# Kernel tuning notes

Measured on AMD Instinct MI355X. Metric: run time of the kernel, lower is better.

Reference implementation:

```python
import jax, jax.numpy as jnp
import numpy as np

N_OBJ = 4096      # n_objects (fixed node count; fc1 consumes flattened node features)
F_IN = 256        # in_feats
H = 256           # n_hidden
C = 128           # n_classes
NE = 8            # number of edge types
EPT = 131072      # edges per etype (avg in-degree 32)


def setup_inputs() -> dict:
    key = jax.random.key(0)
    ks = jax.random.split(key, 16)
    s = 0.02  # weight init scale
    inp = {
        "feat": jax.random.normal(ks[0], (N_OBJ, F_IN), dtype=jnp.float32),
        "edges": jax.random.randint(ks[1], (NE, 2, EPT), 0, N_OBJ, dtype=jnp.int64),
        # 3 hetero layers: layer0 (F_IN->H), layers 1,2 (H->H), each with per-etype Linear
        "W0": jax.random.normal(ks[2], (NE, H, F_IN), dtype=jnp.float32) * s,
        "b0": jnp.zeros((NE, H), dtype=jnp.float32),
        "W1": jax.random.normal(ks[3], (NE, H, H), dtype=jnp.float32) * s,
        "b1": jnp.zeros((NE, H), dtype=jnp.float32),
        "W2": jax.random.normal(ks[4], (NE, H, H), dtype=jnp.float32) * s,
        "b2": jnp.zeros((NE, H), dtype=jnp.float32),
        "fc1_w": jax.random.normal(ks[5], (H, N_OBJ * H), dtype=jnp.float32) * 0.002,
        "fc1_b": jnp.zeros((H,), dtype=jnp.float32),
        "fc2_w": jax.random.normal(ks[6], (C, H), dtype=jnp.float32) * s,
        "fc2_b": jnp.zeros((C,), dtype=jnp.float32),
    }
    return inp


def _hetero_layer(h, W, b, edges):
    # Per-etype linear: Wh[e] = h @ W[e].T + b[e]   -> [NE, N, H]
    Wh = jnp.einsum('nf,ehf->enh', h, W) + b[:, None, :]

    def per_etype(wh, src, dst):
        msg = wh[src]                                            # gather: [EPT, H]
        ssum = jax.ops.segment_sum(msg, dst, num_segments=N_OBJ)  # [N, H]
        deg = jax.ops.segment_sum(jnp.ones_like(dst, dtype=wh.dtype), dst,
                                  num_segments=N_OBJ)             # [N]
        return ssum / jnp.maximum(deg, 1.0)[:, None]              # mean reduce

    agg = jax.vmap(per_etype)(Wh, edges[:, 0], edges[:, 1])  # [NE, N, H]
    # multi_update_all cross-type aggregator 'sum', then activation (relu)
    return jax.nn.relu(agg.sum(axis=0))


def reference(feat, edges, W0, b0, W1, b1, W2, b2, fc1_w, fc1_b, fc2_w, fc2_b):
    h = _hetero_layer(feat, W0, b0, edges)
    h = _hetero_layer(h, W1, b1, edges)
    h = _hetero_layer(h, W2, b2, edges)
    flat = h.reshape(-1)                          # [N*H]
    z = jax.nn.relu(fc1_w @ flat + fc1_b)         # [H]
    out = jax.nn.sigmoid(fc2_w @ z + fc2_b)       # [C]
    return out
```

## Files before the change

### kernel.cpp

```cpp
#include <hip/hip_runtime.h>
#include <math.h>

#define N_OBJ 4096
#define F     256
#define NE    8
#define EPT   131072
#define KCAT  (NE * F)
#define C_OUT 128
#define FC1_K (N_OBJ * F)
#define FCH   16384
#define FNCH  (FC1_K / FCH)
#define FRJ   8

typedef __attribute__((ext_vector_type(8))) short s8v;
typedef __attribute__((ext_vector_type(4))) float f4v;

__device__ inline float bf2f(unsigned short u) {
    unsigned int x = ((unsigned int)u) << 16;
    return __builtin_bit_cast(float, x);
}
__device__ inline unsigned short f2bf(float f) {
    unsigned int x = __builtin_bit_cast(unsigned int, f);
    x += 0x7fff + ((x >> 16) & 1);
    return (unsigned short)(x >> 16);
}
__device__ __forceinline__ int swz(int row, int k8) {
    return (row * 64 + k8 * 8) ^ ((row & 7) << 3);
}


__global__ __launch_bounds__(256) void k_count_deg(const int* __restrict__ edges,
                                                   int* __restrict__ deg) {
    int gid = blockIdx.x * 256 + threadIdx.x;
    int e = gid >> 17;
    int i = gid & (EPT - 1);
    int dst = edges[(e * 2 + 1) * EPT + i];
    atomicAdd(&deg[e * N_OBJ + dst], 1);
}

__global__ __launch_bounds__(256) void k_scan(const int* __restrict__ deg,
                                              int* __restrict__ rowptr,
                                              int* __restrict__ cursor,
                                              float* __restrict__ invdeg) {
    int e = blockIdx.x;
    int t = threadIdx.x;
    __shared__ int part[256];
    int local[16];
    int base = e * N_OBJ + t * 16;
    int s = 0;
#pragma unroll
    for (int i = 0; i < 16; ++i) { local[i] = deg[base + i]; s += local[i]; }
    part[t] = s;
    __syncthreads();
    for (int off = 1; off < 256; off <<= 1) {
        int v = (t >= off) ? part[t - off] : 0;
        __syncthreads();
        part[t] += v;
        __syncthreads();
    }
    int run = part[t] - s;
#pragma unroll
    for (int i = 0; i < 16; ++i) {
        rowptr[base + i] = run;
        cursor[base + i] = run;
        invdeg[base + i] = 1.0f / fmaxf((float)local[i], 1.0f);
        run += local[i];
    }
}

__global__ __launch_bounds__(256) void k_fill(const int* __restrict__ edges,
                                              int* __restrict__ cursor,
                                              int* __restrict__ col) {
    int gid = blockIdx.x * 256 + threadIdx.x;
    int e = gid >> 17;
    int i = gid & (EPT - 1);
    int src = edges[(e * 2 + 0) * EPT + i];
    int dst = edges[(e * 2 + 1) * EPT + i];
    int pos = atomicAdd(&cursor[e * N_OBJ + dst], 1);
    col[e * EPT + pos] = src;
}

__global__ __launch_bounds__(256) void k_bmask(const int* __restrict__ deg,
                                               unsigned int* __restrict__ bmask) {
    int n = blockIdx.x * 256 + threadIdx.x;
    unsigned int m = 0;
#pragma unroll
    for (int e = 0; e < NE; ++e) m |= (deg[e * N_OBJ + n] > 0) ? (1u << e) : 0u;
    bmask[n] = m;
}

#define WQ4 (NE * F * F / 4)
#define FQ4 (N_OBJ * F / 4)
__global__ __launch_bounds__(256) void k_cvt_all(const float* __restrict__ W0,
                                                 const float* __restrict__ W1,
                                                 const float* __restrict__ W2,
                                                 const float* __restrict__ feat,
                                                 unsigned short* __restrict__ Wb0,
                                                 unsigned short* __restrict__ Wb1,
                                                 unsigned short* __restrict__ Wb2,
                                                 unsigned short* __restrict__ featb) {
    int i = blockIdx.x * 256 + threadIdx.x;
    const float* s;
    unsigned short* d;
    int j;
    if (i < WQ4)            { s = W0;   d = Wb0;   j = i; }
    else if (i < 2 * WQ4)   { s = W1;   d = Wb1;   j = i - WQ4; }
    else if (i < 3 * WQ4)   { s = W2;   d = Wb2;   j = i - 2 * WQ4; }
    else                    { s = feat; d = featb; j = i - 3 * WQ4; }
    float4 v = ((const float4*)s)[j];
    ushort4 o;
    o.x = f2bf(v.x); o.y = f2bf(v.y); o.z = f2bf(v.z); o.w = f2bf(v.w);
    ((ushort4*)d)[j] = o;
}

__global__ __launch_bounds__(256) void k_aggregate(const unsigned short* __restrict__ h_in,
                                                   const int* __restrict__ rowptr,
                                                   const int* __restrict__ deg,
                                                   const int* __restrict__ col,
                                                   const float* __restrict__ invdeg,
                                                   unsigned short* __restrict__ ah) {
    int wid = blockIdx.x * 4 + (threadIdx.x >> 6);
    int lane = threadIdx.x & 63;
    int e = wid >> 12;
    int n = wid & (N_OBJ - 1);
    int beg = rowptr[wid];
    int cnt = deg[wid];
    const int* cl = col + e * EPT + beg;
    const ushort4* h4 = (const ushort4*)h_in;
    float a0 = 0.f, a1 = 0.f, a2 = 0.f, a3 = 0.f;
    int k = 0;
    for (; k + 8 <= cnt; k += 8) {
        int s0 = cl[k],     s1 = cl[k + 1], s2 = cl[k + 2], s3 = cl[k + 3];
        int s4 = cl[k + 4], s5 = cl[k + 5], s6 = cl[k + 6], s7 = cl[k + 7];
        ushort4 v0 = h4[s0 * 64 + lane];
        ushort4 v1 = h4[s1 * 64 + lane];
        ushort4 v2 = h4[s2 * 64 + lane];
        ushort4 v3 = h4[s3 * 64 + lane];
        ushort4 v4 = h4[s4 * 64 + lane];
        ushort4 v5 = h4[s5 * 64 + lane];
        ushort4 v6 = h4[s6 * 64 + lane];
        ushort4 v7 = h4[s7 * 64 + lane];
        a0 += bf2f(v0.x) + bf2f(v1.x) + bf2f(v2.x) + bf2f(v3.x)
            + bf2f(v4.x) + bf2f(v5.x) + bf2f(v6.x) + bf2f(v7.x);
        a1 += bf2f(v0.y) + bf2f(v1.y) + bf2f(v2.y) + bf2f(v3.y)
            + bf2f(v4.y) + bf2f(v5.y) + bf2f(v6.y) + bf2f(v7.y);
        a2 += bf2f(v0.z) + bf2f(v1.z) + bf2f(v2.z) + bf2f(v3.z)
            + bf2f(v4.z) + bf2f(v5.z) + bf2f(v6.z) + bf2f(v7.z);
        a3 += bf2f(v0.w) + bf2f(v1.w) + bf2f(v2.w) + bf2f(v3.w)
            + bf2f(v4.w) + bf2f(v5.w) + bf2f(v6.w) + bf2f(v7.w);
    }
    for (; k < cnt; ++k) {
        ushort4 v = h4[cl[k] * 64 + lane];
        a0 += bf2f(v.x); a1 += bf2f(v.y); a2 += bf2f(v.z); a3 += bf2f(v.w);
    }
    float sc = invdeg[wid];
    ushort4 o;
    o.x = f2bf(a0 * sc); o.y = f2bf(a1 * sc); o.z = f2bf(a2 * sc); o.w = f2bf(a3 * sc);
    ((ushort4*)ah)[n * (KCAT / 4) + e * (F / 4) + lane] = o;
}

template <int OUTBF>
__global__ __launch_bounds__(256, 4) void k_gemm(const unsigned short* __restrict__ A,
                                                 const unsigned short* __restrict__ Wb,
                                                 const float* __restrict__ bias,
                                                 const unsigned int* __restrict__ bmask,
                                                 void* __restrict__ Cout) {
    __shared__ short As[2][64 * 64];
    __shared__ short Bs[2][64 * 64];
    int m0 = blockIdx.x * 64, n0 = blockIdx.y * 64;
    int t = threadIdx.x;
    int wave = t >> 6, lane = t & 63;
    int r = lane & 15, g = lane >> 4;
    int row0 = t >> 3, seg0 = t & 7;
    int row1 = row0 + 32;
    int wA0 = swz(row0, seg0), wA1 = swz(row1, seg0);

    const short* Ap = (const short*)A;
    const short* Wp = (const short*)Wb;
    const short* arp0 = Ap + (size_t)(m0 + row0) * KCAT + seg0 * 8;
    const short* arp1 = Ap + (size_t)(m0 + row1) * KCAT + seg0 * 8;
    int brow0 = (n0 + row0) * F + seg0 * 8;
    int brow1 = (n0 + row1) * F + seg0 * 8;

    f4v acc[4];
#pragma unroll
    for (int i = 0; i < 4; ++i) acc[i] = (f4v){0.f, 0.f, 0.f, 0.f};

    {
        s8v a0 = *(const s8v*)(arp0);
        s8v a1 = *(const s8v*)(arp1);
        s8v b0 = *(const s8v*)(Wp + brow0);
        s8v b1 = *(const s8v*)(Wp + brow1);
        *(s8v*)&As[0][wA0] = a0; *(s8v*)&As[0][wA1] = a1;
        *(s8v*)&Bs[0][wA0] = b0; *(s8v*)&Bs[0][wA1] = b1;
    }
    __syncthreads();
#pragma unroll 1
    for (int ks = 0; ks < 32; ++ks) {
        int cur = ks & 1;
        s8v a0, a1, b0, b1;
        if (ks < 31) {
            int kb = (ks + 1) * 64;
            int woff = ((kb >> 8) << 16) + (kb & 255);
            a0 = *(const s8v*)(arp0 + kb);
            a1 = *(const s8v*)(arp1 + kb);
            b0 = *(const s8v*)(Wp + woff + brow0);
            b1 = *(const s8v*)(Wp + woff + brow1);
        }
        const short* as = As[cur];
        const short* bs = Bs[cur];
#pragma unroll
        for (int kk = 0; kk < 2; ++kk) {
            s8v af = *(const s8v*)&as[swz(wave * 16 + r, kk * 4 + g)];
#pragma unroll
            for (int n = 0; n < 4; ++n) {
                s8v bf = *(const s8v*)&bs[swz(n * 16 + r, kk * 4 + g)];
                acc[n] = __builtin_amdgcn_mfma_f32_16x16x32_bf16(af, bf, acc[n], 0, 0, 0);
            }
        }
        if (ks < 31) {
            *(s8v*)&As[cur ^ 1][wA0] = a0; *(s8v*)&As[cur ^ 1][wA1] = a1;
            *(s8v*)&Bs[cur ^ 1][wA0] = b0; *(s8v*)&Bs[cur ^ 1][wA1] = b1;
        }
        __syncthreads();
    }
    int mb = m0 + wave * 16 + g * 4;
    unsigned int msk[4];
#pragma unroll
    for (int reg = 0; reg < 4; ++reg) msk[reg] = bmask[mb + reg];
#pragma unroll
    for (int n = 0; n < 4; ++n) {
        int coln = n0 + n * 16 + r;
        float bcol[NE];
#pragma unroll
        for (int e = 0; e < NE; ++e) bcol[e] = bias[e * F + coln];
#pragma unroll
        for (int reg = 0; reg < 4; ++reg) {
            float v = acc[n][reg];
#pragma unroll
            for (int e = 0; e < NE; ++e)
                if ((msk[reg] >> e) & 1) v += bcol[e];
            v = fmaxf(v, 0.f);
            if (OUTBF) ((unsigned short*)Cout)[(size_t)(mb + reg) * F + coln] = f2bf(v);
            else       ((float*)Cout)[(size_t)(mb + reg) * F + coln] = v;
        }
    }
}

__global__ __launch_bounds__(256) void k_fc1(const float* __restrict__ Wf,
                                             const float* __restrict__ flat,
                                             float* __restrict__ zpart) {
    __shared__ float xs[FCH];
    int c = blockIdx.x;
    int jg = blockIdx.y;
    int t = threadIdx.x;
    const float4* fp = (const float4*)(flat + (size_t)c * FCH);
    float4* xs4 = (float4*)xs;
#pragma unroll
    for (int q = 0; q < FCH / 4 / 256; ++q) xs4[q * 256 + t] = fp[q * 256 + t];
    __syncthreads();
    float accs[FRJ];
#pragma unroll
    for (int rr = 0; rr < FRJ; ++rr) {
        const float4* wp = (const float4*)(Wf + (size_t)(jg * FRJ + rr) * FC1_K
                                              + (size_t)c * FCH);
        float s = 0.0f;
#pragma unroll 4
        for (int it = 0; it < FCH / 4 / 256; ++it) {
            int q = it * 256 + t;
            float4 w4 = wp[q];
            float4 x4 = xs4[q];
            s = fmaf(w4.x, x4.x,
                fmaf(w4.y, x4.y,
                fmaf(w4.z, x4.z,
                fmaf(w4.w, x4.w, s))));
        }
        accs[rr] = s;
    }
    __shared__ float red[4][FRJ];
    int lane = t & 63, wv = t >> 6;
#pragma unroll
    for (int rr = 0; rr < FRJ; ++rr) {
        float s = accs[rr];
#pragma unroll
        for (int off = 32; off > 0; off >>= 1) s += __shfl_down(s, off, 64);
        if (lane == 0) red[wv][rr] = s;
    }
    __syncthreads();
    if (t < FRJ) {
        float s = red[0][t] + red[1][t] + red[2][t] + red[3][t];
        zpart[c * 256 + jg * FRJ + t] = s;
    }
}

__global__ __launch_bounds__(256) void k_final(const float* __restrict__ zpart,
                                               const float* __restrict__ fc1_b,
                                               const float* __restrict__ fc2_w,
                                               const float* __restrict__ fc2_b,
                                               float* __restrict__ out) {
    __shared__ float z[256];
    int t = threadIdx.x;
    float s = fc1_b[t];
#pragma unroll
    for (int c = 0; c < FNCH; ++c) s += zpart[c * 256 + t];
    z[t] = fmaxf(s, 0.0f);
    __syncthreads();
    if (t < C_OUT) {
        float acc = fc2_b[t];
        for (int k = 0; k < 256; ++k) acc = fmaf(fc2_w[t * 256 + k], z[k], acc);
        out[t] = 1.0f / (1.0f + expf(-acc));
    }
}

extern "C" void kernel_launch(void* const* d_in, const int* in_sizes, int n_in,
                              void* d_out, int out_size, void* d_ws, size_t ws_size,
                              hipStream_t stream) {
    const float* feat  = (const float*)d_in[0];
    const int*   edges = (const int*)d_in[1];
    const float* W0    = (const float*)d_in[2];
    const float* b0    = (const float*)d_in[3];
    const float* W1    = (const float*)d_in[4];
    const float* b1    = (const float*)d_in[5];
    const float* W2    = (const float*)d_in[6];
    const float* b2    = (const float*)d_in[7];
    const float* fc1_w = (const float*)d_in[8];
    const float* fc1_b = (const float*)d_in[9];
    const float* fc2_w = (const float*)d_in[10];
    const float* fc2_b = (const float*)d_in[11];
    float* out = (float*)d_out;

    char* ws = (char*)d_ws;
    size_t off = 0;
    auto alloc = [&](size_t bytes) {
        void* p = ws + off;
        off = (off + bytes + 255) & ~(size_t)255;
        return p;
    };
    int*            deg    = (int*)            alloc(NE * N_OBJ * 4);
    int*            rowptr = (int*)            alloc(NE * N_OBJ * 4);
    int*            cursor = (int*)            alloc(NE * N_OBJ * 4);
    float*          invdeg = (float*)          alloc(NE * N_OBJ * 4);
    int*            col    = (int*)            alloc(NE * EPT * 4);
    unsigned int*   bmask  = (unsigned int*)   alloc(N_OBJ * 4);
    float*          zpart  = (float*)          alloc(FNCH * 256 * 4);
    unsigned short* Wb0    = (unsigned short*) alloc((size_t)NE * F * F * 2);
    unsigned short* Wb1    = (unsigned short*) alloc((size_t)NE * F * F * 2);
    unsigned short* Wb2    = (unsigned short*) alloc((size_t)NE * F * F * 2);
    unsigned short* featb  = (unsigned short*) alloc((size_t)N_OBJ * F * 2);
    unsigned short* h_ba   = (unsigned short*) alloc((size_t)N_OBJ * F * 2);
    unsigned short* h_bb   = (unsigned short*) alloc((size_t)N_OBJ * F * 2);
    float*          h_f32  = (float*)          alloc((size_t)N_OBJ * F * 4);
    unsigned short* ah     = (unsigned short*) alloc((size_t)N_OBJ * KCAT * 2);
    (void)ws_size; (void)in_sizes; (void)n_in; (void)out_size;

    hipMemsetAsync(deg, 0, NE * N_OBJ * 4, stream);
    k_count_deg<<<NE * EPT / 256, 256, 0, stream>>>(edges, deg);
    k_scan<<<NE, 256, 0, stream>>>(deg, rowptr, cursor, invdeg);
    k_fill<<<NE * EPT / 256, 256, 0, stream>>>(edges, cursor, col);
    k_bmask<<<N_OBJ / 256, 256, 0, stream>>>(deg, bmask);
    k_cvt_all<<<(3 * WQ4 + FQ4) / 256, 256, 0, stream>>>(W0, W1, W2, feat,
                                                         Wb0, Wb1, Wb2, featb);

    dim3 ggrid(N_OBJ / 64, F / 64);
    int agrid = NE * N_OBJ / 4;

    k_aggregate<<<agrid, 256, 0, stream>>>(featb, rowptr, deg, col, invdeg, ah);
    k_gemm<1><<<ggrid, 256, 0, stream>>>(ah, Wb0, b0, bmask, h_ba);
    k_aggregate<<<agrid, 256, 0, stream>>>(h_ba, rowptr, deg, col, invdeg, ah);
    k_gemm<1><<<ggrid, 256, 0, stream>>>(ah, Wb1, b1, bmask, h_bb);
    k_aggregate<<<agrid, 256, 0, stream>>>(h_bb, rowptr, deg, col, invdeg, ah);
    k_gemm<0><<<ggrid, 256, 0, stream>>>(ah, Wb2, b2, bmask, h_f32);

    dim3 fgrid(FNCH, 256 / FRJ);
    k_fc1<<<fgrid, 256, 0, stream>>>(fc1_w, h_f32, zpart);
    k_final<<<1, 256, 0, stream>>>(zpart, fc1_b, fc2_w, fc2_b, out);
}
```

Before: 484.8 us.

## Halve GEMM M-tile to 32 rows and fold bmask build into scan

The GEMM block tile changes from 64x64 to 32x64, which doubles the grid to 512 blocks. Each wave now owns one 16-column B fragment and reuses it across two 16-row A fragments. The aim is more blocks in flight to fill the GPU's many compute units on this fairly small GEMM, at the cost of loading each B tile twice as often. Separately, the bmask kernel launch is removed: k_scan sets the mask bits with atomicOr, and the memset is extended to zero bmask, which now sits right after deg.

```diff
diff --git a/kernel.cpp b/kernel.cpp
--- a/kernel.cpp
+++ b/kernel.cpp
@@ -41,7 +41,8 @@
 __global__ __launch_bounds__(256) void k_scan(const int* __restrict__ deg,
                                               int* __restrict__ rowptr,
                                               int* __restrict__ cursor,
-                                              float* __restrict__ invdeg) {
+                                              float* __restrict__ invdeg,
+                                              unsigned int* __restrict__ bmask) {
     int e = blockIdx.x;
     int t = threadIdx.x;
     __shared__ int part[256];
@@ -64,6 +65,7 @@
         rowptr[base + i] = run;
         cursor[base + i] = run;
         invdeg[base + i] = 1.0f / fmaxf((float)local[i], 1.0f);
+        if (local[i] > 0) atomicOr(&bmask[t * 16 + i], 1u << e);
         run += local[i];
     }
 }
@@ -78,15 +80,6 @@
     int dst = edges[(e * 2 + 1) * EPT + i];
     int pos = atomicAdd(&cursor[e * N_OBJ + dst], 1);
     col[e * EPT + pos] = src;
-}
-
-__global__ __launch_bounds__(256) void k_bmask(const int* __restrict__ deg,
-                                               unsigned int* __restrict__ bmask) {
-    int n = blockIdx.x * 256 + threadIdx.x;
-    unsigned int m = 0;
-#pragma unroll
-    for (int e = 0; e < NE; ++e) m |= (deg[e * N_OBJ + n] > 0) ? (1u << e) : 0u;
-    bmask[n] = m;
 }
 
 #define WQ4 (NE * F * F / 4)
@@ -165,45 +158,41 @@
                                                  const float* __restrict__ bias,
                                                  const unsigned int* __restrict__ bmask,
                                                  void* __restrict__ Cout) {
-    __shared__ short As[2][64 * 64];
+    __shared__ short As[2][32 * 64];
     __shared__ short Bs[2][64 * 64];
-    int m0 = blockIdx.x * 64, n0 = blockIdx.y * 64;
+    int m0 = blockIdx.x * 32, n0 = blockIdx.y * 64;
     int t = threadIdx.x;
     int wave = t >> 6, lane = t & 63;
     int r = lane & 15, g = lane >> 4;
     int row0 = t >> 3, seg0 = t & 7;
-    int row1 = row0 + 32;
-    int wA0 = swz(row0, seg0), wA1 = swz(row1, seg0);
+    int wA0 = swz(row0, seg0), wA1 = swz(row0 + 32, seg0);
 
     const short* Ap = (const short*)A;
     const short* Wp = (const short*)Wb;
-    const short* arp0 = Ap + (size_t)(m0 + row0) * KCAT + seg0 * 8;
-    const short* arp1 = Ap + (size_t)(m0 + row1) * KCAT + seg0 * 8;
+    const short* arp = Ap + (size_t)(m0 + row0) * KCAT + seg0 * 8;
     int brow0 = (n0 + row0) * F + seg0 * 8;
-    int brow1 = (n0 + row1) * F + seg0 * 8;
-
-    f4v acc[4];
-#pragma unroll
-    for (int i = 0; i < 4; ++i) acc[i] = (f4v){0.f, 0.f, 0.f, 0.f};
+    int brow1 = (n0 + row0 + 32) * F + seg0 * 8;
+
+    f4v acc[2];
+#pragma unroll
+    for (int i = 0; i < 2; ++i) acc[i] = (f4v){0.f, 0.f, 0.f, 0.f};
 
     {
-        s8v a0 = *(const s8v*)(arp0);
-        s8v a1 = *(const s8v*)(arp1);
+        s8v a0 = *(const s8v*)(arp);
         s8v b0 = *(const s8v*)(Wp + brow0);
         s8v b1 = *(const s8v*)(Wp + brow1);
-        *(s8v*)&As[0][wA0] = a0; *(s8v*)&As[0][wA1] = a1;
+        *(s8v*)&As[0][wA0] = a0;
         *(s8v*)&Bs[0][wA0] = b0; *(s8v*)&Bs[0][wA1] = b1;
     }
     __syncthreads();
 #pragma unroll 1
     for (int ks = 0; ks < 32; ++ks) {
         int cur = ks & 1;
-        s8v a0, a1, b0, b1;
+        s8v a0, b0, b1;
         if (ks < 31) {
             int kb = (ks + 1) * 64;
             int woff = ((kb >> 8) << 16) + (kb & 255);
-            a0 = *(const s8v*)(arp0 + kb);
-            a1 = *(const s8v*)(arp1 + kb);
+            a0 = *(const s8v*)(arp + kb);
             b0 = *(const s8v*)(Wp + woff + brow0);
             b1 = *(const s8v*)(Wp + woff + brow1);
         }
@@ -211,38 +200,36 @@
         const short* bs = Bs[cur];
 #pragma unroll
         for (int kk = 0; kk < 2; ++kk) {
-            s8v af = *(const s8v*)&as[swz(wave * 16 + r, kk * 4 + g)];
-#pragma unroll
-            for (int n = 0; n < 4; ++n) {
-                s8v bf = *(const s8v*)&bs[swz(n * 16 + r, kk * 4 + g)];
-                acc[n] = __builtin_amdgcn_mfma_f32_16x16x32_bf16(af, bf, acc[n], 0, 0, 0);
+            s8v bf = *(const s8v*)&bs[swz(wave * 16 + r, kk * 4 + g)];
+#pragma unroll
+            for (int mf = 0; mf < 2; ++mf) {
+                s8v af = *(const s8v*)&as[swz(mf * 16 + r, kk * 4 + g)];
+                acc[mf] = __builtin_amdgcn_mfma_f32_16x16x32_bf16(af, bf, acc[mf], 0, 0, 0);
             }
         }
         if (ks < 31) {
-            *(s8v*)&As[cur ^ 1][wA0] = a0; *(s8v*)&As[cur ^ 1][wA1] = a1;
+            *(s8v*)&As[cur ^ 1][wA0] = a0;
             *(s8v*)&Bs[cur ^ 1][wA0] = b0; *(s8v*)&Bs[cur ^ 1][wA1] = b1;
         }
         __syncthreads();
     }
-    int mb = m0 + wave * 16 + g * 4;
-    unsigned int msk[4];
-#pragma unroll
-    for (int reg = 0; reg < 4; ++reg) msk[reg] = bmask[mb + reg];
-#pragma unroll
-    for (int n = 0; n < 4; ++n) {
-        int coln = n0 + n * 16 + r;
-        float bcol[NE];
-#pragma unroll
-        for (int e = 0; e < NE; ++e) bcol[e] = bias[e * F + coln];
+    int coln = n0 + wave * 16 + r;
+    float bcol[NE];
+#pragma unroll
+    for (int e = 0; e < NE; ++e) bcol[e] = bias[e * F + coln];
+#pragma unroll
+    for (int mf = 0; mf < 2; ++mf) {
 #pragma unroll
         for (int reg = 0; reg < 4; ++reg) {
-            float v = acc[n][reg];
+            int mm = m0 + mf * 16 + g * 4 + reg;
+            unsigned int msk = bmask[mm];
+            float v = acc[mf][reg];
 #pragma unroll
             for (int e = 0; e < NE; ++e)
-                if ((msk[reg] >> e) & 1) v += bcol[e];
+                if ((msk >> e) & 1) v += bcol[e];
             v = fmaxf(v, 0.f);
-            if (OUTBF) ((unsigned short*)Cout)[(size_t)(mb + reg) * F + coln] = f2bf(v);
-            else       ((float*)Cout)[(size_t)(mb + reg) * F + coln] = v;
+            if (OUTBF) ((unsigned short*)Cout)[(size_t)mm * F + coln] = f2bf(v);
+            else       ((float*)Cout)[(size_t)mm * F + coln] = v;
         }
     }
 }
@@ -337,11 +324,11 @@
         return p;
     };
     int*            deg    = (int*)            alloc(NE * N_OBJ * 4);
+    unsigned int*   bmask  = (unsigned int*)   alloc(N_OBJ * 4);
     int*            rowptr = (int*)            alloc(NE * N_OBJ * 4);
     int*            cursor = (int*)            alloc(NE * N_OBJ * 4);
     float*          invdeg = (float*)          alloc(NE * N_OBJ * 4);
     int*            col    = (int*)            alloc(NE * EPT * 4);
-    unsigned int*   bmask  = (unsigned int*)   alloc(N_OBJ * 4);
     float*          zpart  = (float*)          alloc(FNCH * 256 * 4);
     unsigned short* Wb0    = (unsigned short*) alloc((size_t)NE * F * F * 2);
     unsigned short* Wb1    = (unsigned short*) alloc((size_t)NE * F * F * 2);
@@ -353,15 +340,14 @@
     unsigned short* ah     = (unsigned short*) alloc((size_t)N_OBJ * KCAT * 2);
     (void)ws_size; (void)in_sizes; (void)n_in; (void)out_size;
 
-    hipMemsetAsync(deg, 0, NE * N_OBJ * 4, stream);
+    hipMemsetAsync(deg, 0, NE * N_OBJ * 4 + N_OBJ * 4, stream);
     k_count_deg<<<NE * EPT / 256, 256, 0, stream>>>(edges, deg);
-    k_scan<<<NE, 256, 0, stream>>>(deg, rowptr, cursor, invdeg);
+    k_scan<<<NE, 256, 0, stream>>>(deg, rowptr, cursor, invdeg, bmask);
     k_fill<<<NE * EPT / 256, 256, 0, stream>>>(edges, cursor, col);
-    k_bmask<<<N_OBJ / 256, 256, 0, stream>>>(deg, bmask);
     k_cvt_all<<<(3 * WQ4 + FQ4) / 256, 256, 0, stream>>>(W0, W1, W2, feat,
                                                          Wb0, Wb1, Wb2, featb);
 
-    dim3 ggrid(N_OBJ / 64, F / 64);
+    dim3 ggrid(N_OBJ / 32, F / 64);
     int agrid = NE * N_OBJ / 4;
 
     k_aggregate<<<agrid, 256, 0, stream>>>(featb, rowptr, deg, col, invdeg, ah);
```

Measured after the change: 488.5 us. Within noise of the previous version (+0.8%).
